# Performance work log

Measured on AMD Instinct MI355X. Metric: run time of the kernel, lower is better.

The kernel has to match this reference:

```python
import jax, jax.numpy as jnp
import numpy as np

B, N, D, H = 8, 2048, 768, 64

def setup_inputs() -> dict:
    key = jax.random.key(0)
    k1, k2, k3, k4 = jax.random.split(key, 4)
    return {
        "input": jax.random.normal(k1, (B, N, D), dtype=jnp.float32),
        "Wq": jax.random.normal(k2, (D, H), dtype=jnp.float32) * (D ** -0.5),
        "Wk": jax.random.normal(k3, (D, H), dtype=jnp.float32) * (D ** -0.5),
        "Wv": jax.random.normal(k4, (D, H), dtype=jnp.float32) * (D ** -0.5),
    }

def reference(input, Wq, Wk, Wv):
    # Projections: [B, N, H]
    Q = jnp.einsum('bnd,dh->bnh', input, Wq)
    K = jnp.einsum('bnd,dh->bnh', input, Wk)
    V = jnp.einsum('bnd,dh->bnh', input, Wv)
    # Raw scores [B, N, N]; mask BEFORE scaling (as in original; -inf/scale == -inf)
    scores = jnp.einsum('bqh,bkh->bqk', Q, K)
    n = input.shape[1]
    causal = jnp.tril(jnp.ones((n, n), dtype=bool))
    scores = jnp.where(causal, scores, -jnp.inf)
    scores = scores / (K.shape[-1] ** 0.5)
    attn = jax.nn.softmax(scores, axis=-1)
    # dropout_rate=0 -> identity (eval mode)
    return jnp.einsum('bqk,bkh->bqh', attn, V)
```

## Files before the change

### kernel.cpp

```cpp
#include <hip/hip_runtime.h>
#include <stdint.h>

typedef __bf16 bf16_t;
typedef __bf16 bf16x8 __attribute__((ext_vector_type(8)));
typedef float floatx4 __attribute__((ext_vector_type(4)));
typedef float floatx16 __attribute__((ext_vector_type(16)));

#define B_ 8
#define N_ 2048
#define D_ 768
#define H_ 64

#define WAIT_VM0()   { __builtin_amdgcn_sched_barrier(0); __builtin_amdgcn_s_waitcnt(0x0F70); __builtin_amdgcn_sched_barrier(0); }
#define WAIT_LGKM0() { __builtin_amdgcn_sched_barrier(0); __builtin_amdgcn_s_waitcnt(0xC07F); __builtin_amdgcn_sched_barrier(0); }

__device__ __forceinline__ bf16_t f2bf(float f) {
    union { float f; uint32_t u; } v; v.f = f;
    uint32_t u = v.u;
    uint32_t r = (u + 0x7fffu + ((u >> 16) & 1u)) >> 16;
    union { unsigned short s; bf16_t b; } o; o.s = (unsigned short)r;
    return o.b;
}

__device__ __forceinline__ uint32_t pkbf(float lo, float hi_) {
    union { bf16_t b[2]; uint32_t u; } t;
    t.b[0] = f2bf(lo); t.b[1] = f2bf(hi_);
    return t.u;
}

__device__ __forceinline__ void async_cp16(void* l, const void* g) {
    __builtin_amdgcn_global_load_lds(
        (const __attribute__((address_space(1))) uint32_t*)g,
        (__attribute__((address_space(3))) uint32_t*)l, 16, 0, 0);
}

__global__ void wt_kernel(const float* __restrict__ Wq,
                          const float* __restrict__ Wk,
                          const float* __restrict__ Wv,
                          bf16_t* __restrict__ Wt) {
    const int h = threadIdx.x;
    const int k = blockIdx.x;
    const int s = blockIdx.y;
    const float* W = (s == 0) ? Wq : (s == 1) ? Wk : Wv;
    float v = W[k * H_ + h];
    if (s == 0) v *= 0.125f * 1.4426950408889634f;
    Wt[(size_t)(s * 64 + h) * D_ + k] = f2bf(v);
}

__launch_bounds__(256, 4)
__global__ void proj_kernel(const float* __restrict__ X,
                            const bf16_t* __restrict__ Wt,
                            bf16_t* __restrict__ Qb,
                            bf16_t* __restrict__ Kb,
                            bf16_t* __restrict__ Vt) {
    const int wave = threadIdx.x >> 6;
    const int lane = threadIdx.x & 63;
    const int quad = lane >> 4;
    const int l16  = lane & 15;
    const int rowhalf = wave & 1;
    const int colhalf = wave >> 1;
    const int nb = blockIdx.x & 1;
    const int colbase = nb * 96;
    const int m0blk = (blockIdx.x >> 1) * 32;

    __shared__ __align__(16) float  As[2][32 * 64];
    __shared__ __align__(16) bf16_t Bs[2][96 * 64];

    floatx4 acc[3];
#pragma unroll
    for (int i = 0; i < 3; i++) acc[i] = (floatx4){0.f, 0.f, 0.f, 0.f};

    auto stage = [&](int buf, int k0) {
#pragma unroll
        for (int i = 0; i < 2; i++) {
            const int r = (wave * 2 + i) * 4 + (lane >> 4);
            const int c = (lane & 15) ^ (r & 15);
            const float* g = X + (size_t)(m0blk + r) * D_ + k0 + c * 4;
            async_cp16((char*)&As[buf][0] + (wave * 2 + i) * 1024, g);
        }
#pragma unroll
        for (int i = 0; i < 3; i++) {
            const int r = (wave * 3 + i) * 8 + (lane >> 3);
            const int c = (lane & 7) ^ (r & 7);
            const bf16_t* g = Wt + (size_t)(colbase + r) * D_ + k0 + c * 8;
            async_cp16((char*)&Bs[buf][0] + (wave * 3 + i) * 1024, g);
        }
    };

    const int arow = rowhalf * 16 + l16;

    stage(0, 0);
    for (int ch = 0; ch < 12; ch++) {
        __syncthreads();
        if (ch + 1 < 12) stage((ch + 1) & 1, (ch + 1) * 64);

        const char* Ab = (const char*)&As[ch & 1][0];
        const char* Bb = (const char*)&Bs[ch & 1][0];
#pragma unroll
        for (int kh = 0; kh < 2; kh++) {
            const int c0 = kh * 8 + quad * 2;
            float4 xa = *(const float4*)(Ab + arow * 256 + ((c0 ^ l16) & 15) * 16);
            float4 xb = *(const float4*)(Ab + arow * 256 + (((c0 + 1) ^ l16) & 15) * 16);
            bf16x8 af;
            af[0] = f2bf(xa.x); af[1] = f2bf(xa.y);
            af[2] = f2bf(xa.z); af[3] = f2bf(xa.w);
            af[4] = f2bf(xb.x); af[5] = f2bf(xb.y);
            af[6] = f2bf(xb.z); af[7] = f2bf(xb.w);
            const int cb = kh * 4 + quad;
#pragma unroll
            for (int nt = 0; nt < 3; nt++) {
                const int nl = colhalf * 48 + nt * 16 + l16;
                bf16x8 bf = *(const bf16x8*)(Bb + nl * 128 + ((cb ^ (nl & 7))) * 16);
                acc[nt] = __builtin_amdgcn_mfma_f32_16x16x32_bf16(af, bf, acc[nt], 0, 0, 0);
            }
        }
    }

#pragma unroll
    for (int nt = 0; nt < 3; nt++) {
        const int c = colbase + colhalf * 48 + nt * 16 + l16;
#pragma unroll
        for (int r = 0; r < 4; r++) {
            const int m = m0blk + rowhalf * 16 + quad * 4 + r;
            bf16_t val = f2bf(acc[nt][r]);
            if (c < 64) {
                Qb[(size_t)m * H_ + c] = val;
            } else if (c < 128) {
                Kb[(size_t)m * H_ + (c - 64)] = val;
            } else {
                const int b = m >> 11, n = m & 2047, h = c - 128;
                Vt[((size_t)b * H_ + h) * N_ + n] = val;
            }
        }
    }
}

__launch_bounds__(512, 4)
__global__ void attn_kernel(const bf16_t* __restrict__ Qb,
                            const bf16_t* __restrict__ Kb,
                            const bf16_t* __restrict__ Vt,
                            float* __restrict__ Out) {
    const int x = blockIdx.x;
    const int b = blockIdx.y;
    const int z = blockIdx.z;
    const int qt = z ? (63 - x) : x;
    const int q0 = qt * 32;

    const int tid  = threadIdx.x;
    const int wave = tid >> 6;
    const int lane = tid & 63;
    const int hi   = lane >> 5;
    const int lq   = lane & 31;

    __shared__ __align__(16) char smem[8 * 8192 + 1024];
    char* mybase = smem + wave * 8192;
    float* Ol = (float*)smem;
    float* Ll = (float*)(smem + 65536);

    const bf16_t* KpB = Kb + (size_t)b * N_ * H_;
    const bf16_t* VpB = Vt + (size_t)b * H_ * N_;

    const bf16_t* qrow = Qb + ((size_t)b * N_ + q0 + lq) * H_ + hi * 8;
    bf16x8 qf0 = *(const bf16x8*)(qrow);
    bf16x8 qf1 = *(const bf16x8*)(qrow + 16);
    bf16x8 qf2 = *(const bf16x8*)(qrow + 32);
    bf16x8 qf3 = *(const bf16x8*)(qrow + 48);

    floatx16 o0, o1;
#pragma unroll
    for (int i = 0; i < 16; i++) { o0[i] = 0.f; o1[i] = 0.f; }
    float ls = 0.f;

    const int rK = lane >> 3, cK = lane & 7;
    auto stage_k = [&](int k0, char* buf) {
#pragma unroll
        for (int i = 0; i < 4; i++) {
            const int r = i * 8 + rK;
            const int mk = rK ^ ((i & 1) << 2);
            async_cp16(buf + i * 1024,
                       KpB + (size_t)(k0 + r) * H_ + (cK ^ mk) * 8);
        }
    };

    const int ktm = qt;
    if (wave <= ktm)     stage_k(wave * 32, mybase);
    if (wave + 8 <= ktm) stage_k((wave + 8) * 32, mybase + 4096);

    const int mK = (lq & 7) ^ ((lq & 8) >> 1);

    for (int kt = wave; kt <= ktm; kt += 8) {
        const int k0 = kt * 32;
        char* kb = mybase + (((kt - wave) >> 3) & 1) * 4096;

        if (kt == wave) { WAIT_VM0(); }

        bf16x8 kf0 = *(const bf16x8*)(kb + lq * 128 + (((0 + hi) ^ mK) * 16));
        bf16x8 kf1 = *(const bf16x8*)(kb + lq * 128 + (((2 + hi) ^ mK) * 16));
        bf16x8 kf2 = *(const bf16x8*)(kb + lq * 128 + (((4 + hi) ^ mK) * 16));
        bf16x8 kf3 = *(const bf16x8*)(kb + lq * 128 + (((6 + hi) ^ mK) * 16));
        WAIT_LGKM0();

        const bf16_t* vrow0 = VpB + (size_t)lq * N_ + k0 + 8 * hi;
        const bf16_t* vrow1 = vrow0 + (size_t)32 * N_;
        bf16x8 vf00 = *(const bf16x8*)(vrow0);
        bf16x8 vf01 = *(const bf16x8*)(vrow0 + 16);
        bf16x8 vf10 = *(const bf16x8*)(vrow1);
        bf16x8 vf11 = *(const bf16x8*)(vrow1 + 16);
        __builtin_amdgcn_sched_barrier(0);
        if (kt + 16 <= ktm) stage_k(k0 + 512, kb);

        floatx16 st;
#pragma unroll
        for (int i = 0; i < 16; i++) st[i] = 0.f;
        st = __builtin_amdgcn_mfma_f32_32x32x16_bf16(kf0, qf0, st, 0, 0, 0);
        st = __builtin_amdgcn_mfma_f32_32x32x16_bf16(kf1, qf1, st, 0, 0, 0);
        st = __builtin_amdgcn_mfma_f32_32x32x16_bf16(kf2, qf2, st, 0, 0, 0);
        st = __builtin_amdgcn_mfma_f32_32x32x16_bf16(kf3, qf3, st, 0, 0, 0);

        if (kt < qt) {
#pragma unroll
            for (int r = 0; r < 16; r++) st[r] = exp2f(st[r]);
        } else {
#pragma unroll
            for (int r = 0; r < 16; r++) {
                const int row = (r & 3) + 8 * (r >> 2) + 4 * hi;
                st[r] = (row <= lq) ? exp2f(st[r]) : 0.f;
            }
        }
#pragma unroll
        for (int r = 0; r < 16; r++) ls += st[r];

        uint32_t pb[8];
#pragma unroll
        for (int t = 0; t < 8; t++) pb[t] = pkbf(st[2 * t], st[2 * t + 1]);
        uint32_t rc[4];
#pragma unroll
        for (int t = 0; t < 4; t++) {
            const uint32_t w = hi ? pb[(t & 1) + 4 * (t >> 1)]
                                  : pb[(t & 1) + 2 + 4 * (t >> 1)];
            rc[t] = (uint32_t)__shfl_xor((int)w, 32, 64);
        }
        union { uint32_t u[4]; bf16x8 v; } f0, f1;
        f0.u[0] = hi ? rc[0] : pb[0]; f0.u[1] = hi ? rc[1] : pb[1];
        f0.u[2] = hi ? pb[2] : rc[0]; f0.u[3] = hi ? pb[3] : rc[1];
        f1.u[0] = hi ? rc[2] : pb[4]; f1.u[1] = hi ? rc[3] : pb[5];
        f1.u[2] = hi ? pb[6] : rc[2]; f1.u[3] = hi ? pb[7] : rc[3];

        o0 = __builtin_amdgcn_mfma_f32_32x32x16_bf16(f0.v, vf00, o0, 0, 0, 0);
        o0 = __builtin_amdgcn_mfma_f32_32x32x16_bf16(f1.v, vf01, o0, 0, 0, 0);
        o1 = __builtin_amdgcn_mfma_f32_32x32x16_bf16(f0.v, vf10, o1, 0, 0, 0);
        o1 = __builtin_amdgcn_mfma_f32_32x32x16_bf16(f1.v, vf11, o1, 0, 0, 0);
    }

    float lst = ls + __shfl_xor(ls, 32, 64);
    __syncthreads();
    if (hi == 0) Ll[wave * 32 + lq] = lst;
#pragma unroll
    for (int r = 0; r < 16; r++) {
        const int q = (r & 3) + 8 * (r >> 2) + 4 * hi;
        Ol[((size_t)wave * 32 + q) * 64 + lq]      = o0[r];
        Ol[((size_t)wave * 32 + q) * 64 + 32 + lq] = o1[r];
    }
    __syncthreads();
    {
        const int q  = tid >> 4;
        const int h4 = (tid & 15) * 4;
        floatx4 a = (floatx4){0.f, 0.f, 0.f, 0.f};
        float l = 0.f;
#pragma unroll
        for (int w = 0; w < 8; w++) {
            const floatx4 part = *(const floatx4*)&Ol[((size_t)w * 32 + q) * 64 + h4];
            a += part;
            l += Ll[w * 32 + q];
        }
        const float inv = 1.0f / l;
        float4 outv = {a[0] * inv, a[1] * inv, a[2] * inv, a[3] * inv};
        *(float4*)&Out[((size_t)b * N_ + q0 + q) * H_ + h4] = outv;
    }
}

extern "C" void kernel_launch(void* const* d_in, const int* in_sizes, int n_in,
                              void* d_out, int out_size, void* d_ws, size_t ws_size,
                              hipStream_t stream) {
    const float* X  = (const float*)d_in[0];
    const float* Wq = (const float*)d_in[1];
    const float* Wk = (const float*)d_in[2];
    const float* Wv = (const float*)d_in[3];
    float* Out = (float*)d_out;

    char* ws = (char*)d_ws;
    bf16_t* Qb = (bf16_t*)(ws);
    bf16_t* Kb = (bf16_t*)(ws + (size_t)(2u << 20));
    bf16_t* Vt = (bf16_t*)(ws + (size_t)(4u << 20));
    bf16_t* Wt = (bf16_t*)(ws + (size_t)(6u << 20));

    hipLaunchKernelGGL(wt_kernel, dim3(768, 3), dim3(64), 0, stream, Wq, Wk, Wv, Wt);
    hipLaunchKernelGGL(proj_kernel, dim3(1024), dim3(256), 0, stream, X, Wt, Qb, Kb, Vt);
    hipLaunchKernelGGL(attn_kernel, dim3(32, 8, 2), dim3(512), 0, stream, Qb, Kb, Vt, Out);
}
```

Measured before the change: 120.9 us.

## Widen projection block to all 192 columns, use native bf16 casts

The projection kernel now runs 512-thread blocks, each covering all 192 output columns (Q, K and V) for a 32-row tile. Previously two blocks split the columns and each read the same fp32 X tile, so X, the largest input, is now fetched from global memory once instead of twice. Manual bit-twiddling float-to-bf16 rounding is replaced with the native bf16 cast, which can lower to hardware conversion instructions. The softmax row-sum accumulation becomes a tree reduction to shorten the dependency chain. The larger LDS footprint and block size may reduce occupancy in the projection kernel.

Result: faster. 113.9 us (-5.8%).

```diff
diff --git a/kernel.cpp b/kernel.cpp
--- a/kernel.cpp
+++ b/kernel.cpp
@@ -15,16 +15,12 @@
 #define WAIT_LGKM0() { __builtin_amdgcn_sched_barrier(0); __builtin_amdgcn_s_waitcnt(0xC07F); __builtin_amdgcn_sched_barrier(0); }
 
 __device__ __forceinline__ bf16_t f2bf(float f) {
-    union { float f; uint32_t u; } v; v.f = f;
-    uint32_t u = v.u;
-    uint32_t r = (u + 0x7fffu + ((u >> 16) & 1u)) >> 16;
-    union { unsigned short s; bf16_t b; } o; o.s = (unsigned short)r;
-    return o.b;
+    return (bf16_t)f;
 }
 
 __device__ __forceinline__ uint32_t pkbf(float lo, float hi_) {
     union { bf16_t b[2]; uint32_t u; } t;
-    t.b[0] = f2bf(lo); t.b[1] = f2bf(hi_);
+    t.b[0] = (bf16_t)lo; t.b[1] = (bf16_t)hi_;
     return t.u;
 }
 
@@ -47,7 +43,7 @@
     Wt[(size_t)(s * 64 + h) * D_ + k] = f2bf(v);
 }
 
-__launch_bounds__(256, 4)
+__launch_bounds__(512, 4)
 __global__ void proj_kernel(const float* __restrict__ X,
                             const bf16_t* __restrict__ Wt,
                             bf16_t* __restrict__ Qb,
@@ -57,32 +53,29 @@
     const int lane = threadIdx.x & 63;
     const int quad = lane >> 4;
     const int l16  = lane & 15;
-    const int rowhalf = wave & 1;
-    const int colhalf = wave >> 1;
-    const int nb = blockIdx.x & 1;
-    const int colbase = nb * 96;
-    const int m0blk = (blockIdx.x >> 1) * 32;
+    const int rowhalf = wave >> 2;
+    const int colq    = wave & 3;
+    const int m0blk = blockIdx.x * 32;
 
     __shared__ __align__(16) float  As[2][32 * 64];
-    __shared__ __align__(16) bf16_t Bs[2][96 * 64];
+    __shared__ __align__(16) bf16_t Bs[2][192 * 64];
 
     floatx4 acc[3];
 #pragma unroll
     for (int i = 0; i < 3; i++) acc[i] = (floatx4){0.f, 0.f, 0.f, 0.f};
 
     auto stage = [&](int buf, int k0) {
-#pragma unroll
-        for (int i = 0; i < 2; i++) {
-            const int r = (wave * 2 + i) * 4 + (lane >> 4);
+        {
+            const int r = wave * 4 + (lane >> 4);
             const int c = (lane & 15) ^ (r & 15);
             const float* g = X + (size_t)(m0blk + r) * D_ + k0 + c * 4;
-            async_cp16((char*)&As[buf][0] + (wave * 2 + i) * 1024, g);
+            async_cp16((char*)&As[buf][0] + wave * 1024, g);
         }
 #pragma unroll
         for (int i = 0; i < 3; i++) {
             const int r = (wave * 3 + i) * 8 + (lane >> 3);
             const int c = (lane & 7) ^ (r & 7);
-            const bf16_t* g = Wt + (size_t)(colbase + r) * D_ + k0 + c * 8;
+            const bf16_t* g = Wt + (size_t)r * D_ + k0 + c * 8;
             async_cp16((char*)&Bs[buf][0] + (wave * 3 + i) * 1024, g);
         }
     };
@@ -109,7 +102,7 @@
             const int cb = kh * 4 + quad;
 #pragma unroll
             for (int nt = 0; nt < 3; nt++) {
-                const int nl = colhalf * 48 + nt * 16 + l16;
+                const int nl = colq * 48 + nt * 16 + l16;
                 bf16x8 bf = *(const bf16x8*)(Bb + nl * 128 + ((cb ^ (nl & 7))) * 16);
                 acc[nt] = __builtin_amdgcn_mfma_f32_16x16x32_bf16(af, bf, acc[nt], 0, 0, 0);
             }
@@ -118,7 +111,7 @@
 
 #pragma unroll
     for (int nt = 0; nt < 3; nt++) {
-        const int c = colbase + colhalf * 48 + nt * 16 + l16;
+        const int c = colq * 48 + nt * 16 + l16;
 #pragma unroll
         for (int r = 0; r < 4; r++) {
             const int m = m0blk + rowhalf * 16 + quad * 4 + r;
@@ -227,8 +220,13 @@
                 st[r] = (row <= lq) ? exp2f(st[r]) : 0.f;
             }
         }
-#pragma unroll
-        for (int r = 0; r < 16; r++) ls += st[r];
+        {
+            float t0 = (st[0] + st[1]) + (st[2] + st[3]);
+            float t1 = (st[4] + st[5]) + (st[6] + st[7]);
+            float t2 = (st[8] + st[9]) + (st[10] + st[11]);
+            float t3 = (st[12] + st[13]) + (st[14] + st[15]);
+            ls += (t0 + t1) + (t2 + t3);
+        }
 
         uint32_t pb[8];
 #pragma unroll
@@ -295,6 +293,6 @@
     bf16_t* Wt = (bf16_t*)(ws + (size_t)(6u << 20));
 
     hipLaunchKernelGGL(wt_kernel, dim3(768, 3), dim3(64), 0, stream, Wq, Wk, Wv, Wt);
-    hipLaunchKernelGGL(proj_kernel, dim3(1024), dim3(256), 0, stream, X, Wt, Qb, Kb, Vt);
+    hipLaunchKernelGGL(proj_kernel, dim3(512), dim3(512), 0, stream, X, Wt, Qb, Kb, Vt);
     hipLaunchKernelGGL(attn_kernel, dim3(32, 8, 2), dim3(512), 0, stream, Qb, Kb, Vt, Out);
 }
```
